# Kernel tuning notes

Measured on AMD Instinct MI355X. Metric: run time of the kernel, lower is better.

The kernel has to match this reference:

```python
import jax, jax.numpy as jnp
import numpy as np

B, S, H = 32, 255, 1024
BS, WD, O = 120, 20, 10
HSZ = 2 * (BS + 1) + WD  # 262


def setup_inputs() -> dict:
    key = jax.random.key(0)
    ks = jax.random.split(key, 9)
    inv = lambda *d: 1.0 / np.sqrt(d[0])
    return {
        "state": jax.random.normal(ks[0], (B, S, H), jnp.float32),
        "head_w": jax.random.normal(ks[1], (H, BS), jnp.float32) * inv(H),
        "head_b": jax.random.normal(ks[2], (BS,), jnp.float32) * 0.02,
        "tail_w": jax.random.normal(ks[3], (H, BS), jnp.float32) * inv(H),
        "tail_b": jax.random.normal(ks[4], (BS,), jnp.float32) * 0.02,
        "U": jax.random.normal(ks[5], (O, BS, BS), jnp.float32) * inv(BS),
        "width_table": jax.random.normal(ks[6], (256, WD), jnp.float32).at[0].set(0.0),  # padding_idx=0
        "cls_w": jax.random.normal(ks[7], (O, HSZ), jnp.float32) * inv(HSZ),
        "cls_b": jax.random.normal(ks[8], (O,), jnp.float32) * 0.02,
    }


def _leaky_relu(x):
    return jnp.where(x >= 0, x, 0.01 * x)  # torch LeakyReLU default slope


def reference(state, head_w, head_b, tail_w, tail_b, U, width_table, cls_w, cls_b):
    b, s, _ = state.shape
    bs = head_w.shape[1]
    # head/tail MLPs (dropout is identity in eval)
    h = _leaky_relu(state @ head_w + head_b)  # (b, s, bs)
    t = _leaky_relu(state @ tail_w + tail_b)  # (b, s, bs)

    # bilinear term
    scores1 = jnp.einsum('bxi,oij,byj->bxyo', h, U, t)  # (b, s, s, O)

    # append bias-ones feature
    ones = jnp.ones((b, s, 1), h.dtype)
    h1 = jnp.concatenate([h, ones], axis=-1)  # (b, s, bs+1)
    t1 = jnp.concatenate([t, ones], axis=-1)

    # span-width embedding: pos[x, y] = y - x + 1, clamped to 0 for y < x
    pos = jnp.arange(s)[None, :] - jnp.arange(s)[:, None] + 1
    pos = pos * (pos > 0)
    wemb = width_table[pos]  # (s, s, WD)

    # cls(concat(h1_x, t1_y, wemb_xy)) decomposed into three small projections
    # + broadcast-add; mathematically identical to materializing affined_cat.
    Wh = cls_w[:, :bs + 1]              # (O, bs+1)
    Wt = cls_w[:, bs + 1:2 * (bs + 1)]  # (O, bs+1)
    Ww = cls_w[:, 2 * (bs + 1):]        # (O, WD)
    scores2 = (jnp.einsum('bxi,oi->bxo', h1, Wh)[:, :, None, :]
               + jnp.einsum('byi,oi->byo', t1, Wt)[:, None, :, :]
               + jnp.einsum('xyw,ow->xyo', wemb, Ww)[None]
               + cls_b)
    return scores1 + scores2
```

## Files before the change

kernel.cpp:

```cpp
#include <hip/hip_runtime.h>
#include <hip/hip_bf16.h>

using f32x4 = __attribute__((ext_vector_type(4))) float;
using f32x2 = __attribute__((ext_vector_type(2))) float;
using s16x8 = __attribute__((ext_vector_type(8))) short;
using s16x4 = __attribute__((ext_vector_type(4))) short;

constexpr int S = 255, RTOT = 32 * 255;
constexpr int NHW = 8160 * 12;

__device__ inline unsigned short f2bf(float x) {
    __hip_bfloat16 b = __float2bfloat16(x);
    return __builtin_bit_cast(unsigned short, b);
}
__device__ inline float bf2f(unsigned short u) {
    unsigned int t = ((unsigned int)u) << 16;
    return __builtin_bit_cast(float, t);
}
__device__ inline f32x4 mfma16(s16x8 a, s16x8 b, f32x4 c) {
    return __builtin_amdgcn_mfma_f32_16x16x32_bf16(a, b, c, 0, 0, 0);
}
__device__ inline void gload16(const unsigned short* g, unsigned short* l) {
    __builtin_amdgcn_global_load_lds(
        (const __attribute__((address_space(1))) void*)g,
        (__attribute__((address_space(3))) void*)l, 16, 0, 0);
}

__global__ __launch_bounds__(256) void convert_k(
    const float* __restrict__ head_w, const float* __restrict__ tail_w,
    const float* __restrict__ U,
    unsigned short* __restrict__ WP, unsigned short* __restrict__ Ut)
{
    int gid = blockIdx.x * 256 + threadIdx.x;
    if (gid < 262144) {
        int e = gid & 7, kcp = (gid >> 3) & 7, n = (gid >> 6) & 255, ks = gid >> 14;
        int kc = kcp ^ (n & 7);
        int k = ks * 64 + kc * 8 + e;
        float v;
        if (n < 128) v = (n < 120) ? head_w[k * 120 + n] : 0.f;
        else { int nn = n - 128; v = (nn < 120) ? tail_w[k * 120 + nn] : 0.f; }
        WP[gid] = f2bf(v);
    } else {
        int idx = gid - 262144;
        if (idx < 163840) {
            int o = idx >> 14, rem = idx & 16383;
            int j = rem >> 7, i2 = rem & 127;
            float v = (i2 < 120 && j < 120) ? U[((size_t)o * 120 + i2) * 120 + j] : 0.f;
            Ut[(size_t)o * 16384 + (size_t)j * 128 + i2] = f2bf(v);
        }
    }
}

__global__ __launch_bounds__(256) void ht_mfma(
    const float* __restrict__ state, const unsigned short* __restrict__ WP,
    const float* __restrict__ head_b, const float* __restrict__ tail_b,
    unsigned short* __restrict__ hbuf, unsigned short* __restrict__ tbuf)
{
    __shared__ unsigned short Ss[2][32 * 64];
    __shared__ unsigned short Ws[2][256 * 64];
    const int r0 = blockIdx.x * 32;
    const int tid = threadIdx.x;
    const int w = tid >> 6, lane = tid & 63;
    const int l16 = lane & 15, kq = lane >> 4;
    const int srow = tid >> 3, skc = tid & 7;
    const float* sp = &state[(size_t)(r0 + srow) * 1024 + skc * 8];

    f32x4 acc[4][2];
    #pragma unroll
    for (int fn = 0; fn < 4; ++fn)
        #pragma unroll
        for (int fr = 0; fr < 2; ++fr) acc[fn][fr] = (f32x4){0.f, 0.f, 0.f, 0.f};

    #pragma unroll
    for (int j = 0; j < 8; ++j) {
        int off = (w * 8 + j) * 512;
        gload16(WP + off + lane * 8, &Ws[0][off]);
    }
    {
        f32x4 a0 = *(const f32x4*)sp;
        f32x4 a1 = *(const f32x4*)(sp + 4);
        s16x8 pk;
        #pragma unroll
        for (int e = 0; e < 4; ++e) { pk[e] = (short)f2bf(a0[e]); pk[e + 4] = (short)f2bf(a1[e]); }
        *(s16x8*)((char*)&Ss[0][0] + srow * 128 + ((skc * 16) ^ ((srow & 7) << 4))) = pk;
    }
    __syncthreads();

    for (int it = 0; it < 16; ++it) {
        const int cur = it & 1;
        f32x4 a0, a1;
        if (it < 15) {
            #pragma unroll
            for (int j = 0; j < 8; ++j) {
                int off = (w * 8 + j) * 512;
                gload16(WP + (it + 1) * 16384 + off + lane * 8, &Ws[cur ^ 1][off]);
            }
            a0 = *(const f32x4*)(sp + (it + 1) * 64);
            a1 = *(const f32x4*)(sp + (it + 1) * 64 + 4);
        }
        const char* SsB = (const char*)&Ss[cur][0];
        const char* WsB = (const char*)&Ws[cur][0];
        s16x8 bf[2][2];
        #pragma unroll
        for (int fr = 0; fr < 2; ++fr) {
            int rr = fr * 16 + l16;
            #pragma unroll
            for (int ks = 0; ks < 2; ++ks)
                bf[fr][ks] = *(const s16x8*)(SsB + rr * 128 + ((ks * 64 + kq * 16) ^ ((rr & 7) << 4)));
        }
        #pragma unroll
        for (int fn = 0; fn < 4; ++fn) {
            int n = w * 64 + fn * 16 + l16;
            #pragma unroll
            for (int ks = 0; ks < 2; ++ks) {
                s16x8 af = *(const s16x8*)(WsB + n * 128 + ((ks * 64 + kq * 16) ^ ((n & 7) << 4)));
                #pragma unroll
                for (int fr = 0; fr < 2; ++fr)
                    acc[fn][fr] = mfma16(af, bf[fr][ks], acc[fn][fr]);
            }
        }
        if (it < 15) {
            s16x8 pk;
            #pragma unroll
            for (int e = 0; e < 4; ++e) { pk[e] = (short)f2bf(a0[e]); pk[e + 4] = (short)f2bf(a1[e]); }
            *(s16x8*)((char*)&Ss[cur ^ 1][0] + srow * 128 + ((skc * 16) ^ ((srow & 7) << 4))) = pk;
        }
        __syncthreads();
    }

    #pragma unroll
    for (int fn = 0; fn < 4; ++fn) {
        const int n0 = w * 64 + fn * 16 + kq * 4;
        const int isT = n0 >= 128;
        const int c0 = n0 & 127;
        const float* bp = isT ? tail_b : head_b;
        unsigned short* dst = isT ? tbuf : hbuf;
        #pragma unroll
        for (int fr = 0; fr < 2; ++fr) {
            const int r = r0 + fr * 16 + l16;
            s16x4 pk;
            #pragma unroll
            for (int e = 0; e < 4; ++e) {
                float bv = (c0 + e < 120) ? bp[c0 + e] : 0.f;
                float z = acc[fn][fr][e] + bv;
                z = (z >= 0.f) ? z : 0.01f * z;
                pk[e] = (short)f2bf(z);
            }
            *(s16x4*)&dst[(size_t)r * 128 + c0] = pk;
        }
    }
}

__global__ __launch_bounds__(256) void hU_mfma(
    const unsigned short* __restrict__ hbuf, const unsigned short* __restrict__ Ut,
    unsigned short* __restrict__ hU)
{
    __shared__ unsigned short Hs[128 * 128];
    __shared__ unsigned short Us[128 * 128];
    const int r0 = blockIdx.x * 128;
    const int o = blockIdx.y;
    const int tid = threadIdx.x;
    const int w = tid >> 6, lane = tid & 63;
    const int l16 = lane & 15, kq = lane >> 4;
    char* HsB = (char*)Hs;
    char* UsB = (char*)Us;

    #pragma unroll
    for (int i = 0; i < 8; ++i) {
        int idx = i * 256 + tid;
        int row = idx >> 4, kc = idx & 15;
        int r = r0 + row;
        s16x8 pk = {0, 0, 0, 0, 0, 0, 0, 0};
        if (r < RTOT) pk = *(const s16x8*)&hbuf[(size_t)r * 128 + kc * 8];
        *(s16x8*)(HsB + row * 256 + ((kc * 16) ^ ((row & 7) << 4))) = pk;
        s16x8 pu = *(const s16x8*)&Ut[(size_t)o * 16384 + (size_t)row * 128 + kc * 8];
        *(s16x8*)(UsB + row * 256 + ((kc * 16) ^ ((row & 7) << 4))) = pu;
    }
    __syncthreads();

    f32x4 acc[2][8];
    #pragma unroll
    for (int a = 0; a < 2; ++a)
        #pragma unroll
        for (int b2 = 0; b2 < 8; ++b2) acc[a][b2] = (f32x4){0.f, 0.f, 0.f, 0.f};

    #pragma unroll
    for (int ks = 0; ks < 4; ++ks) {
        int kb = ks * 64 + kq * 16;
        s16x8 bf[2];
        #pragma unroll
        for (int fr = 0; fr < 2; ++fr) {
            int row = w * 32 + fr * 16 + l16;
            bf[fr] = *(const s16x8*)(HsB + row * 256 + (kb ^ ((row & 7) << 4)));
        }
        #pragma unroll
        for (int fj = 0; fj < 8; ++fj) {
            int j = fj * 16 + l16;
            s16x8 af = *(const s16x8*)(UsB + j * 256 + (kb ^ ((j & 7) << 4)));
            #pragma unroll
            for (int fr = 0; fr < 2; ++fr)
                acc[fr][fj] = mfma16(af, bf[fr], acc[fr][fj]);
        }
    }

    #pragma unroll
    for (int fr = 0; fr < 2; ++fr) {
        int r = r0 + w * 32 + fr * 16 + l16;
        if (r < RTOT) {
            #pragma unroll
            for (int fj = 0; fj < 8; ++fj) {
                int j0 = fj * 16 + kq * 4;
                s16x4 pk;
                #pragma unroll
                for (int e = 0; e < 4; ++e) pk[e] = (short)f2bf(acc[fr][fj][e]);
                *(s16x4*)&hU[((size_t)r * 12 + o) * 128 + j0] = pk;
            }
        }
    }
}

__global__ __launch_bounds__(256) void small_k(
    const unsigned short* __restrict__ hbuf, const unsigned short* __restrict__ tbuf,
    const float* __restrict__ wtab, const float* __restrict__ cls_w,
    const float* __restrict__ cls_b,
    float* __restrict__ hwp, float* __restrict__ twp, float* __restrict__ tblp)
{
    const int gid = blockIdx.x * 256 + threadIdx.x;
    if (gid < 2 * NHW) {
        int which = gid >= NHW;
        int rem = which ? gid - NHW : gid;
        int r = rem / 12, o = rem % 12;
        float s = 0.f;
        if (o < 10) {
            const unsigned short* src = (which ? tbuf : hbuf) + (size_t)r * 128;
            const float* wrow = cls_w + o * 262 + which * 121;
            #pragma unroll
            for (int c = 0; c < 15; ++c) {
                s16x8 v = *(const s16x8*)&src[c * 8];
                #pragma unroll
                for (int e = 0; e < 8; ++e)
                    s += bf2f((unsigned short)v[e]) * wrow[c * 8 + e];
            }
            s += wrow[120];
            if (!which) s += cls_b[o];
        }
        if (which) twp[rem] = s; else hwp[rem] = s;
    } else {
        int id = gid - 2 * NHW;
        if (id < 256 * 12) {
            int p = id / 12, o = id % 12;
            float s = 0.f;
            if (o < 10) {
                for (int wq = 0; wq < 20; ++wq)
                    s += wtab[p * 20 + wq] * cls_w[o * 262 + 242 + wq];
            }
            tblp[id] = s;
        }
    }
}

__global__ __launch_bounds__(512) void main_mfma(
    const unsigned short* __restrict__ hU, const unsigned short* __restrict__ tbuf,
    const float* __restrict__ hwp, const float* __restrict__ twp,
    const float* __restrict__ tblp, float* __restrict__ out)
{
    __shared__ unsigned short Bs[256 * 128];
    __shared__ unsigned short As[2][128 * 128];
    const int mg = blockIdx.x, b = blockIdx.y;
    const int tid = threadIdx.x;
    const int w = tid >> 6, lane = tid & 63;
    const int l16 = lane & 15, kq = lane >> 4;
    const int wm = w >> 2, wy = w & 3;
    const size_t hUbase = (size_t)b * 3060 * 128;

    #pragma unroll
    for (int j = 0; j < 8; ++j) {
        int E = (w * 8 + j) * 512 + lane * 8;
        int row = E >> 7, kcp = (E & 127) >> 3;
        int kc = kcp ^ (row & 7);
        gload16(&tbuf[(size_t)(b * 255 + row) * 128 + kc * 8], &Bs[(w * 8 + j) * 512]);
    }
    {
        const int m0 = mg * 3 * 128;
        #pragma unroll
        for (int j = 0; j < 4; ++j) {
            int E = (w * 4 + j) * 512 + lane * 8;
            int row = E >> 7, kcp = (E & 127) >> 3;
            int kc = kcp ^ (row & 7);
            gload16(&hU[hUbase + (size_t)(m0 + row) * 128 + kc * 8], &As[0][(w * 4 + j) * 512]);
        }
    }
    __syncthreads();

    s16x8 bfr[4][4];
    #pragma unroll
    for (int ks = 0; ks < 4; ++ks)
        #pragma unroll
        for (int fy = 0; fy < 4; ++fy) {
            int row = wy * 64 + fy * 16 + l16;
            bfr[ks][fy] = *(const s16x8*)((const char*)Bs + row * 256 +
                           ((ks * 64 + kq * 16) ^ ((row & 7) << 4)));
        }

    for (int i = 0; i < 3; ++i) {
        const int m0 = (mg * 3 + i) * 128;
        if (i < 2) {
            const int m0n = (mg * 3 + i + 1) * 128;
            #pragma unroll
            for (int j = 0; j < 4; ++j) {
                int E = (w * 4 + j) * 512 + lane * 8;
                int row = E >> 7, kcp = (E & 127) >> 3;
                int kc = kcp ^ (row & 7);
                gload16(&hU[hUbase + (size_t)(m0n + row) * 128 + kc * 8],
                        &As[(i + 1) & 1][(w * 4 + j) * 512]);
            }
        }
        const char* AsB = (const char*)&As[i & 1][0];
        f32x4 acc[4][4];
        #pragma unroll
        for (int fm = 0; fm < 4; ++fm)
            #pragma unroll
            for (int fy = 0; fy < 4; ++fy) acc[fm][fy] = (f32x4){0.f, 0.f, 0.f, 0.f};

        #pragma unroll
        for (int ks = 0; ks < 4; ++ks) {
            s16x8 af[4];
            #pragma unroll
            for (int fm = 0; fm < 4; ++fm) {
                int row = wm * 64 + fm * 16 + l16;
                af[fm] = *(const s16x8*)(AsB + row * 256 +
                          ((ks * 64 + kq * 16) ^ ((row & 7) << 4)));
            }
            #pragma unroll
            for (int fm = 0; fm < 4; ++fm)
                #pragma unroll
                for (int fy = 0; fy < 4; ++fy)
                    acc[fm][fy] = mfma16(af[fm], bfr[ks][fy], acc[fm][fy]);
        }

        #pragma unroll
        for (int fm = 0; fm < 4; ++fm) {
            const int ml = m0 + wm * 64 + fm * 16 + kq * 4;
            if (ml < 3060) {
                const int x = ml / 12, o0 = ml % 12;
                const int rx = b * 255 + x;
                f32x4 hv = *(const f32x4*)&hwp[(size_t)rx * 12 + o0];
                #pragma unroll
                for (int fy = 0; fy < 4; ++fy) {
                    const int y = wy * 64 + fy * 16 + l16;
                    if (y < 255) {
                        const int ry = b * 255 + y;
                        f32x4 tv = *(const f32x4*)&twp[(size_t)ry * 12 + o0];
                        int p = y - x + 1; if (p < 0) p = 0;
                        f32x4 wv = *(const f32x4*)&tblp[p * 12 + o0];
                        float* op = &out[((size_t)rx * 255 + y) * 10 + o0];
                        if (o0 < 8) {
                            float v[4];
                            #pragma unroll
                            for (int e = 0; e < 4; ++e)
                                v[e] = acc[fm][fy][e] + hv[e] + tv[e] + wv[e];
                            __builtin_memcpy(op, v, 16);
                        } else {
                            float v[2];
                            v[0] = acc[fm][fy][0] + hv[0] + tv[0] + wv[0];
                            v[1] = acc[fm][fy][1] + hv[1] + tv[1] + wv[1];
                            __builtin_memcpy(op, v, 8);
                        }
                    }
                }
            }
        }
        __syncthreads();
    }
}

extern "C" void kernel_launch(void* const* d_in, const int* in_sizes, int n_in,
                              void* d_out, int out_size, void* d_ws, size_t ws_size,
                              hipStream_t stream)
{
    (void)in_sizes; (void)n_in; (void)out_size; (void)ws_size;
    const float* state  = (const float*)d_in[0];
    const float* head_w = (const float*)d_in[1];
    const float* head_b = (const float*)d_in[2];
    const float* tail_w = (const float*)d_in[3];
    const float* tail_b = (const float*)d_in[4];
    const float* U      = (const float*)d_in[5];
    const float* wtab   = (const float*)d_in[6];
    const float* cls_w  = (const float*)d_in[7];
    const float* cls_b  = (const float*)d_in[8];
    float* out = (float*)d_out;

    unsigned short* u16 = (unsigned short*)d_ws;
    unsigned short* hbuf = u16;
    unsigned short* tbuf = hbuf + 1044480;
    unsigned short* hUb  = tbuf + 1044480;
    unsigned short* WP   = hUb + 12533760;
    unsigned short* Ut   = WP + 262144;
    float* hwp  = (float*)(Ut + 163840);
    float* twp  = hwp + 97920;
    float* tblp = twp + 97920;

    hipLaunchKernelGGL(convert_k, dim3(1664), dim3(256), 0, stream,
                       head_w, tail_w, U, WP, Ut);
    hipLaunchKernelGGL(ht_mfma, dim3(255), dim3(256), 0, stream,
                       state, WP, head_b, tail_b, hbuf, tbuf);
    hipLaunchKernelGGL(hU_mfma, dim3(64, 10), dim3(256), 0, stream,
                       hbuf, Ut, hUb);
    hipLaunchKernelGGL(small_k, dim3(778), dim3(256), 0, stream,
                       hbuf, tbuf, wtab, cls_w, cls_b, hwp, twp, tblp);
    hipLaunchKernelGGL(main_mfma, dim3(8, 32), dim3(512), 0, stream,
                       hUb, tbuf, hwp, twp, tblp, out);
}
```

Measured before the change: 94.16 us.

## Fuse small projections into producers and pre-swizzle buffers for direct LDS loads

Removes the separate small_k kernel. The width-table projection moves into convert_k, and the per-row h/t classifier projections are computed inside ht_mfma from an LDS copy of the tile it just produced. The h, t, U and hU buffers are now written in an XOR-swizzled, padded layout, so later kernels can use global_load_lds with plain contiguous addresses instead of computing the swizzle on the load side. hU_mfma now uses async LDS loads, and main_mfma moves its barrier to before the epilogue. The cost is extra epilogue work and LDS traffic in ht_mfma, plus padded buffers and one fewer launch.

```diff
diff --git a/kernel.cpp b/kernel.cpp
--- a/kernel.cpp
+++ b/kernel.cpp
@@ -2,12 +2,10 @@
 #include <hip/hip_bf16.h>
 
 using f32x4 = __attribute__((ext_vector_type(4))) float;
-using f32x2 = __attribute__((ext_vector_type(2))) float;
 using s16x8 = __attribute__((ext_vector_type(8))) short;
 using s16x4 = __attribute__((ext_vector_type(4))) short;
 
 constexpr int S = 255, RTOT = 32 * 255;
-constexpr int NHW = 8160 * 12;
 
 __device__ inline unsigned short f2bf(float x) {
     __hip_bfloat16 b = __float2bfloat16(x);
@@ -26,10 +24,13 @@
         (__attribute__((address_space(3))) void*)l, 16, 0, 0);
 }
 
+
 __global__ __launch_bounds__(256) void convert_k(
     const float* __restrict__ head_w, const float* __restrict__ tail_w,
-    const float* __restrict__ U,
-    unsigned short* __restrict__ WP, unsigned short* __restrict__ Ut)
+    const float* __restrict__ U, const float* __restrict__ wtab,
+    const float* __restrict__ cls_w,
+    unsigned short* __restrict__ WP, unsigned short* __restrict__ Ut,
+    float* __restrict__ tblp)
 {
     int gid = blockIdx.x * 256 + threadIdx.x;
     if (gid < 262144) {
@@ -40,13 +41,21 @@
         if (n < 128) v = (n < 120) ? head_w[k * 120 + n] : 0.f;
         else { int nn = n - 128; v = (nn < 120) ? tail_w[k * 120 + nn] : 0.f; }
         WP[gid] = f2bf(v);
+    } else if (gid < 262144 + 163840) {
+        int idx = gid - 262144;
+        int j = idx & 127, i2 = (idx >> 7) & 127, o = idx >> 14;
+        float v = (i2 < 120 && j < 120) ? U[((size_t)o * 120 + i2) * 120 + j] : 0.f;
+        int ph = (((i2 >> 3) ^ (j & 7)) << 3) | (i2 & 7);
+        Ut[(size_t)o * 16384 + (size_t)j * 128 + ph] = f2bf(v);
     } else {
-        int idx = gid - 262144;
-        if (idx < 163840) {
-            int o = idx >> 14, rem = idx & 16383;
-            int j = rem >> 7, i2 = rem & 127;
-            float v = (i2 < 120 && j < 120) ? U[((size_t)o * 120 + i2) * 120 + j] : 0.f;
-            Ut[(size_t)o * 16384 + (size_t)j * 128 + i2] = f2bf(v);
+        int id = gid - 262144 - 163840;
+        if (id < 2560) {
+            int p = id / 10, o = id - (id / 10) * 10;
+            float s = 0.f;
+            #pragma unroll
+            for (int wq = 0; wq < 20; ++wq)
+                s += wtab[p * 20 + wq] * cls_w[o * 262 + 242 + wq];
+            tblp[p * 12 + o] = s;
         }
     }
 }
@@ -54,7 +63,9 @@
 __global__ __launch_bounds__(256) void ht_mfma(
     const float* __restrict__ state, const unsigned short* __restrict__ WP,
     const float* __restrict__ head_b, const float* __restrict__ tail_b,
-    unsigned short* __restrict__ hbuf, unsigned short* __restrict__ tbuf)
+    const float* __restrict__ cls_w, const float* __restrict__ cls_b,
+    unsigned short* __restrict__ hbuf, unsigned short* __restrict__ tbuf,
+    float* __restrict__ hwp, float* __restrict__ twp)
 {
     __shared__ unsigned short Ss[2][32 * 64];
     __shared__ unsigned short Ws[2][256 * 64];
@@ -128,16 +139,19 @@
         __syncthreads();
     }
 
+    unsigned short* Hl = &Ws[0][0];
+    unsigned short* Tl = &Ws[1][0];
     #pragma unroll
     for (int fn = 0; fn < 4; ++fn) {
         const int n0 = w * 64 + fn * 16 + kq * 4;
         const int isT = n0 >= 128;
         const int c0 = n0 & 127;
+        const int g = c0 >> 3, sub = (kq & 1) * 4;
         const float* bp = isT ? tail_b : head_b;
-        unsigned short* dst = isT ? tbuf : hbuf;
         #pragma unroll
         for (int fr = 0; fr < 2; ++fr) {
-            const int r = r0 + fr * 16 + l16;
+            const int rloc = fr * 16 + l16;
+            const int r = r0 + rloc;
             s16x4 pk;
             #pragma unroll
             for (int e = 0; e < 4; ++e) {
@@ -146,8 +160,44 @@
                 z = (z >= 0.f) ? z : 0.01f * z;
                 pk[e] = (short)f2bf(z);
             }
-            *(s16x4*)&dst[(size_t)r * 128 + c0] = pk;
-        }
+            if (isT) {
+                int bq = r / 255, x = r - bq * 255;
+                *(s16x4*)&tbuf[((size_t)bq * 256 + x) * 128 + ((g ^ (x & 7)) << 3) + sub] = pk;
+                *(s16x4*)&Tl[rloc * 128 + c0] = pk;
+            } else {
+                *(s16x4*)&hbuf[(size_t)r * 128 + ((g ^ (r & 7)) << 3) + sub] = pk;
+                *(s16x4*)&Hl[rloc * 128 + c0] = pk;
+            }
+        }
+    }
+    __syncthreads();
+
+    float* Wl = (float*)&Ws[0][4096];
+    for (int idx = tid; idx < 2430; idx += 256) {
+        if (idx < 2420) {
+            int which = idx / 1210, rem = idx - which * 1210;
+            int o = rem / 121, i = rem - o * 121;
+            Wl[idx] = cls_w[o * 262 + which * 121 + i];
+        } else Wl[idx] = cls_b[idx - 2420];
+    }
+    __syncthreads();
+    for (int d = tid; d < 640; d += 256) {
+        int which = d / 320, rem = d - which * 320;
+        int rr = rem / 10, o = rem - rr * 10;
+        const unsigned short* row = (which ? Tl : Hl) + rr * 128;
+        const float* wp2 = &Wl[which * 1210 + o * 121];
+        float s = 0.f;
+        #pragma unroll
+        for (int c = 0; c < 15; ++c) {
+            s16x8 v = *(const s16x8*)&row[c * 8];
+            #pragma unroll
+            for (int e = 0; e < 8; ++e)
+                s += bf2f((unsigned short)v[e]) * wp2[c * 8 + e];
+        }
+        s += wp2[120];
+        int gr = r0 + rr;
+        if (!which) hwp[(size_t)gr * 12 + o] = s + Wl[2420 + o];
+        else        twp[(size_t)gr * 12 + o] = s;
     }
 }
 
@@ -162,19 +212,14 @@
     const int tid = threadIdx.x;
     const int w = tid >> 6, lane = tid & 63;
     const int l16 = lane & 15, kq = lane >> 4;
-    char* HsB = (char*)Hs;
-    char* UsB = (char*)Us;
-
-    #pragma unroll
-    for (int i = 0; i < 8; ++i) {
-        int idx = i * 256 + tid;
-        int row = idx >> 4, kc = idx & 15;
-        int r = r0 + row;
-        s16x8 pk = {0, 0, 0, 0, 0, 0, 0, 0};
-        if (r < RTOT) pk = *(const s16x8*)&hbuf[(size_t)r * 128 + kc * 8];
-        *(s16x8*)(HsB + row * 256 + ((kc * 16) ^ ((row & 7) << 4))) = pk;
-        s16x8 pu = *(const s16x8*)&Ut[(size_t)o * 16384 + (size_t)row * 128 + kc * 8];
-        *(s16x8*)(UsB + row * 256 + ((kc * 16) ^ ((row & 7) << 4))) = pu;
+    const char* HsB = (const char*)Hs;
+    const char* UsB = (const char*)Us;
+
+    #pragma unroll
+    for (int j = 0; j < 8; ++j) {
+        int off = (w * 8 + j) * 512;
+        gload16(&hbuf[(size_t)r0 * 128 + off + lane * 8], &Hs[off]);
+        gload16(&Ut[(size_t)o * 16384 + off + lane * 8], &Us[off]);
     }
     __syncthreads();
 
@@ -207,54 +252,18 @@
     for (int fr = 0; fr < 2; ++fr) {
         int r = r0 + w * 32 + fr * 16 + l16;
         if (r < RTOT) {
+            int bq = r / 255, x = r - bq * 255;
+            int m = x * 12 + o;
+            size_t rowbase = ((size_t)bq * 3072 + m) * 128;
+            int key = m & 7, sub = (kq & 1) * 4;
             #pragma unroll
             for (int fj = 0; fj < 8; ++fj) {
-                int j0 = fj * 16 + kq * 4;
+                int g = fj * 2 + (kq >> 1);
                 s16x4 pk;
                 #pragma unroll
                 for (int e = 0; e < 4; ++e) pk[e] = (short)f2bf(acc[fr][fj][e]);
-                *(s16x4*)&hU[((size_t)r * 12 + o) * 128 + j0] = pk;
-            }
-        }
-    }
-}
-
-__global__ __launch_bounds__(256) void small_k(
-    const unsigned short* __restrict__ hbuf, const unsigned short* __restrict__ tbuf,
-    const float* __restrict__ wtab, const float* __restrict__ cls_w,
-    const float* __restrict__ cls_b,
-    float* __restrict__ hwp, float* __restrict__ twp, float* __restrict__ tblp)
-{
-    const int gid = blockIdx.x * 256 + threadIdx.x;
-    if (gid < 2 * NHW) {
-        int which = gid >= NHW;
-        int rem = which ? gid - NHW : gid;
-        int r = rem / 12, o = rem % 12;
-        float s = 0.f;
-        if (o < 10) {
-            const unsigned short* src = (which ? tbuf : hbuf) + (size_t)r * 128;
-            const float* wrow = cls_w + o * 262 + which * 121;
-            #pragma unroll
-            for (int c = 0; c < 15; ++c) {
-                s16x8 v = *(const s16x8*)&src[c * 8];
-                #pragma unroll
-                for (int e = 0; e < 8; ++e)
-                    s += bf2f((unsigned short)v[e]) * wrow[c * 8 + e];
-            }
-            s += wrow[120];
-            if (!which) s += cls_b[o];
-        }
-        if (which) twp[rem] = s; else hwp[rem] = s;
-    } else {
-        int id = gid - 2 * NHW;
-        if (id < 256 * 12) {
-            int p = id / 12, o = id % 12;
-            float s = 0.f;
-            if (o < 10) {
-                for (int wq = 0; wq < 20; ++wq)
-                    s += wtab[p * 20 + wq] * cls_w[o * 262 + 242 + wq];
-            }
-            tblp[id] = s;
+                *(s16x4*)&hU[rowbase + ((g ^ key) << 3) + sub] = pk;
+            }
         }
     }
 }
@@ -271,23 +280,20 @@
     const int w = tid >> 6, lane = tid & 63;
     const int l16 = lane & 15, kq = lane >> 4;
     const int wm = w >> 2, wy = w & 3;
-    const size_t hUbase = (size_t)b * 3060 * 128;
+    const size_t hUbase = (size_t)b * 3072 * 128;
+    const size_t tbase = (size_t)b * 256 * 128;
 
     #pragma unroll
     for (int j = 0; j < 8; ++j) {
-        int E = (w * 8 + j) * 512 + lane * 8;
-        int row = E >> 7, kcp = (E & 127) >> 3;
-        int kc = kcp ^ (row & 7);
-        gload16(&tbuf[(size_t)(b * 255 + row) * 128 + kc * 8], &Bs[(w * 8 + j) * 512]);
+        int off = (w * 8 + j) * 512;
+        gload16(&tbuf[tbase + off + lane * 8], &Bs[off]);
     }
     {
-        const int m0 = mg * 3 * 128;
+        const size_t a0 = hUbase + (size_t)(mg * 3 * 128) * 128;
         #pragma unroll
         for (int j = 0; j < 4; ++j) {
-            int E = (w * 4 + j) * 512 + lane * 8;
-            int row = E >> 7, kcp = (E & 127) >> 3;
-            int kc = kcp ^ (row & 7);
-            gload16(&hU[hUbase + (size_t)(m0 + row) * 128 + kc * 8], &As[0][(w * 4 + j) * 512]);
+            int off = (w * 4 + j) * 512;
+            gload16(&hU[a0 + off + lane * 8], &As[0][off]);
         }
     }
     __syncthreads();
@@ -305,14 +311,11 @@
     for (int i = 0; i < 3; ++i) {
         const int m0 = (mg * 3 + i) * 128;
         if (i < 2) {
-            const int m0n = (mg * 3 + i + 1) * 128;
+            const size_t an = hUbase + (size_t)(m0 + 128) * 128;
             #pragma unroll
             for (int j = 0; j < 4; ++j) {
-                int E = (w * 4 + j) * 512 + lane * 8;
-                int row = E >> 7, kcp = (E & 127) >> 3;
-                int kc = kcp ^ (row & 7);
-                gload16(&hU[hUbase + (size_t)(m0n + row) * 128 + kc * 8],
-                        &As[(i + 1) & 1][(w * 4 + j) * 512]);
+                int off = (w * 4 + j) * 512;
+                gload16(&hU[an + off + lane * 8], &As[(i + 1) & 1][off]);
             }
         }
         const char* AsB = (const char*)&As[i & 1][0];
@@ -337,6 +340,8 @@
                 for (int fy = 0; fy < 4; ++fy)
                     acc[fm][fy] = mfma16(af[fm], bfr[ks][fy], acc[fm][fy]);
         }
+
+        __syncthreads();
 
         #pragma unroll
         for (int fm = 0; fm < 4; ++fm) {
@@ -370,7 +375,6 @@
                 }
             }
         }
-        __syncthreads();
     }
 }
 
@@ -393,21 +397,20 @@
     unsigned short* u16 = (unsigned short*)d_ws;
     unsigned short* hbuf = u16;
     unsigned short* tbuf = hbuf + 1044480;
-    unsigned short* hUb  = tbuf + 1044480;
-    unsigned short* WP   = hUb + 12533760;
+    unsigned short* hUb  = tbuf + 1048576;
+    unsigned short* WP   = hUb + 12582912;
     unsigned short* Ut   = WP + 262144;
     float* hwp  = (float*)(Ut + 163840);
     float* twp  = hwp + 97920;
     float* tblp = twp + 97920;
 
-    hipLaunchKernelGGL(convert_k, dim3(1664), dim3(256), 0, stream,
-                       head_w, tail_w, U, WP, Ut);
+    hipLaunchKernelGGL(convert_k, dim3(1674), dim3(256), 0, stream,
+                       head_w, tail_w, U, wtab, cls_w, WP, Ut, tblp);
     hipLaunchKernelGGL(ht_mfma, dim3(255), dim3(256), 0, stream,
-                       state, WP, head_b, tail_b, hbuf, tbuf);
+                       state, WP, head_b, tail_b, cls_w, cls_b,
+                       hbuf, tbuf, hwp, twp);
     hipLaunchKernelGGL(hU_mfma, dim3(64, 10), dim3(256), 0, stream,
                        hbuf, Ut, hUb);
-    hipLaunchKernelGGL(small_k, dim3(778), dim3(256), 0, stream,
-                       hbuf, tbuf, wtab, cls_w, cls_b, hwp, twp, tblp);
     hipLaunchKernelGGL(main_mfma, dim3(8, 32), dim3(512), 0, stream,
                        hUb, tbuf, hwp, twp, tblp, out);
 }
```

After: 89.50 us. 1.05x faster.
